# Performance work log

Measured on AMD Instinct MI355X. Metric: run time of the kernel, lower is better.

The kernel has to match this reference:

```python
import jax, jax.numpy as jnp
import numpy as np

NUM_PARTS = 2
SAMPLE_STEP = 3  # models sample_points(pts, 3, True) as deterministic stride-3 subsampling


def quat_to_rot(q):
    # wxyz quaternion -> 3x3 rotation (same formula as the torch module)
    q = q / jnp.linalg.norm(q)
    a, b, c, d = q[0], q[1], q[2], q[3]
    return jnp.stack([
        1 - 2 * c * c - 2 * d * d, 2 * b * c - 2 * a * d, 2 * a * c + 2 * b * d,
        2 * b * c + 2 * a * d, 1 - 2 * b * b - 2 * d * d, 2 * c * d - 2 * a * b,
        2 * b * d - 2 * a * c, 2 * a * b + 2 * c * d, 1 - 2 * b * b - 2 * c * c,
    ]).reshape(3, 3)


def make_transform(q, t):
    rot = quat_to_rot(q)                      # (3,3)
    top = jnp.concatenate([rot, t], axis=1)   # (3,4)
    bottom = jnp.array([[0.0, 0.0, 0.0, 1.0]], dtype=top.dtype)
    return jnp.concatenate([top, bottom], axis=0)  # (4,4)


def chamfer(x, y):
    # x: (M,4), y: (M,4) homogeneous points; symmetric chamfer of Euclidean cdist
    d2 = jnp.sum(x * x, -1)[:, None] + jnp.sum(y * y, -1)[None, :] - 2.0 * (x @ y.T)
    d = jnp.sqrt(jnp.maximum(d2, 0.0))
    return jnp.mean(jnp.min(d, axis=1)) + jnp.mean(jnp.min(d, axis=0))


def setup_inputs() -> dict:
    key = jax.random.key(0)
    ks = jax.random.split(key, 6)
    N = 24576
    camera_pts = jax.random.normal(ks[0], (NUM_PARTS, N, 3), dtype=jnp.float32)
    cad_pts = jax.random.normal(ks[1], (NUM_PARTS, N, 3), dtype=jnp.float32)
    part_weight = jax.random.uniform(ks[2], (NUM_PARTS + 1,), dtype=jnp.float32)
    rot_quat = jax.random.normal(ks[3], (NUM_PARTS, 4), dtype=jnp.float32)
    tra = jax.random.normal(ks[4], (NUM_PARTS, 3, 1), dtype=jnp.float32)
    joint_axes = jax.random.normal(ks[5], (NUM_PARTS, 2, 4), dtype=jnp.float32)
    return {"camera_pts": camera_pts, "cad_pts": cad_pts, "part_weight": part_weight,
            "rot_quat": rot_quat, "tra": tra, "joint_axes": joint_axes}


def reference(camera_pts, cad_pts, part_weight, rot_quat, tra, joint_axes):
    # stride-3 subsample, then homogenize with a ones column
    scad = cad_pts[:, ::SAMPLE_STEP]      # (P, M, 3)
    scam = camera_pts[:, ::SAMPLE_STEP]   # (P, M, 3)
    ones = jnp.ones(scad.shape[:-1] + (1,), dtype=scad.dtype)
    scad_h = jnp.concatenate([scad, ones], axis=-1)  # (P, M, 4)
    scam_h = jnp.concatenate([scam, ones], axis=-1)  # (P, M, 4)

    transforms = jax.vmap(make_transform)(rot_quat, tra)        # (P, 4, 4)
    cad_base = jnp.einsum('pij,pnj->pni', transforms, scad_h)   # (P, M, 4)

    e_geo_parts = jax.vmap(chamfer)(cad_base, scam_h)           # (P,)
    e_geo = jnp.dot(part_weight[:NUM_PARTS], e_geo_parts)

    diff = transforms[0] @ joint_axes[0].T - transforms[1] @ joint_axes[1].T  # (4, K)
    e_kin = jax.nn.sigmoid(-5.0 * jnp.linalg.norm(diff))

    all_objective = e_geo + part_weight[NUM_PARTS] * e_kin
    return all_objective, e_kin, jax.lax.stop_gradient(transforms)
```

## Files before the change

kernel.cpp:

```cpp
#include <hip/hip_runtime.h>
#include <math.h>

#define NS 8192
#define NPTS 24576
#define YSPLIT 16
#define YTILE 512
#define BX 256
#define XPT 4
#define XB (NS / (BX * XPT))


__global__ void prep_kernel(const float* __restrict__ rot_quat,
                            const float* __restrict__ tra,
                            const float* __restrict__ joint_axes,
                            float* __restrict__ ws, float* __restrict__ out) {
    if (threadIdx.x == 0) {
        float T[2][16];
        for (int p = 0; p < 2; ++p) {
            float a = rot_quat[p * 4 + 0], b = rot_quat[p * 4 + 1];
            float c = rot_quat[p * 4 + 2], d = rot_quat[p * 4 + 3];
            float inv = rsqrtf(a * a + b * b + c * c + d * d);
            a *= inv; b *= inv; c *= inv; d *= inv;
            float* t = T[p];
            t[0]  = 1.f - 2.f * c * c - 2.f * d * d;
            t[1]  = 2.f * b * c - 2.f * a * d;
            t[2]  = 2.f * a * c + 2.f * b * d;
            t[3]  = tra[p * 3 + 0];
            t[4]  = 2.f * b * c + 2.f * a * d;
            t[5]  = 1.f - 2.f * b * b - 2.f * d * d;
            t[6]  = 2.f * c * d - 2.f * a * b;
            t[7]  = tra[p * 3 + 1];
            t[8]  = 2.f * b * d - 2.f * a * c;
            t[9]  = 2.f * a * b + 2.f * c * d;
            t[10] = 1.f - 2.f * b * b - 2.f * c * c;
            t[11] = tra[p * 3 + 2];
            t[12] = 0.f; t[13] = 0.f; t[14] = 0.f; t[15] = 1.f;
            for (int k = 0; k < 16; ++k) {
                ws[4 + p * 16 + k] = t[k];
                out[2 + p * 16 + k] = t[k];
            }
        }
        float ss = 0.f;
        for (int i = 0; i < 4; ++i) {
            for (int j = 0; j < 2; ++j) {
                float d0 = 0.f, d1 = 0.f;
                for (int k = 0; k < 4; ++k) {
                    d0 += T[0][i * 4 + k] * joint_axes[0 * 8 + j * 4 + k];
                    d1 += T[1][i * 4 + k] * joint_axes[1 * 8 + j * 4 + k];
                }
                float df = d0 - d1;
                ss += df * df;
            }
        }
        float nrm = sqrtf(ss);
        float ek = 1.f / (1.f + expf(5.f * nrm));
        ws[36] = ek;
        out[1] = ek;
        ws[0] = 0.f; ws[1] = 0.f; ws[2] = 0.f; ws[3] = 0.f;
    }
}

__global__ void pack_kernel(const float* __restrict__ cam_pts,
                            const float* __restrict__ cad_pts,
                            const float* __restrict__ ws,
                            float4* __restrict__ pts) {
    int gid = blockIdx.x * blockDim.x + threadIdx.x;
    if (gid >= 2 * NS) return;
    int p = gid >> 13;
    int i = gid & (NS - 1);
    const float* T = ws + 4 + p * 16;
    int base = p * NPTS * 3 + i * 9;
    float x = cad_pts[base], y = cad_pts[base + 1], z = cad_pts[base + 2];
    float q0 = T[0] * x + T[1] * y + T[2]  * z + T[3];
    float q1 = T[4] * x + T[5] * y + T[6]  * z + T[7];
    float q2 = T[8] * x + T[9] * y + T[10] * z + T[11];
    pts[p * NS + i] = make_float4(q0, q1, q2, q0 * q0 + q1 * q1 + q2 * q2);
    float cx = cam_pts[base], cy = cam_pts[base + 1], cz = cam_pts[base + 2];
    pts[2 * NS + p * NS + i] = make_float4(cx, cy, cz, cx * cx + cy * cy + cz * cz);
}

__global__ __launch_bounds__(BX) void chamfer_kernel(const float4* __restrict__ pts,
                                                     float* __restrict__ partial) {
    int combo = blockIdx.y;
    int p   = combo >> 1;
    int dir = combo & 1;
    const float4* X = pts + (dir == 0 ? p * NS : 2 * NS + p * NS);
    const float4* Y = pts + (dir == 0 ? 2 * NS + p * NS : p * NS);
    int ys = blockIdx.z;
    int xb = blockIdx.x;

    __shared__ float4 sy[YTILE];

    int xbase = xb * (BX * XPT) + threadIdx.x;
    float m0[XPT], m1[XPT], m2[XPT], s[XPT], dmin[XPT];
#pragma unroll
    for (int k = 0; k < XPT; ++k) {
        float4 v = X[xbase + k * BX];
        m0[k] = -2.f * v.x;
        m1[k] = -2.f * v.y;
        m2[k] = -2.f * v.z;
        s[k]  = v.w;
        dmin[k] = 3.4e38f;
    }

    int ybase = ys * YTILE;
    sy[threadIdx.x]       = Y[ybase + threadIdx.x];
    sy[threadIdx.x + BX]  = Y[ybase + BX + threadIdx.x];
    __syncthreads();

#pragma unroll 4
    for (int j = 0; j < YTILE; ++j) {
        float4 y = sy[j];
#pragma unroll
        for (int k = 0; k < XPT; ++k) {
            float d = s[k] + y.w;
            d = fmaf(m0[k], y.x, d);
            d = fmaf(m1[k], y.y, d);
            d = fmaf(m2[k], y.z, d);
            dmin[k] = fminf(dmin[k], d);
        }
    }

#pragma unroll
    for (int k = 0; k < XPT; ++k) {
        partial[combo * (YSPLIT * NS) + ys * NS + xbase + k * BX] = dmin[k];
    }
}

__global__ void reduce_kernel(const float* __restrict__ partial,
                              float* __restrict__ accum) {
    int combo = blockIdx.y;
    int x = blockIdx.x * 256 + threadIdx.x;
    const float* p = partial + combo * (YSPLIT * NS) + x;
    float m = p[0];
#pragma unroll
    for (int ysi = 1; ysi < YSPLIT; ++ysi) m = fminf(m, p[ysi * NS]);
    float d = sqrtf(fmaxf(m, 0.f));
#pragma unroll
    for (int off = 32; off > 0; off >>= 1) d += __shfl_down(d, off, 64);
    __shared__ float sm[4];
    int wid = threadIdx.x >> 6;
    if ((threadIdx.x & 63) == 0) sm[wid] = d;
    __syncthreads();
    if (threadIdx.x == 0) {
        float sum = sm[0] + sm[1] + sm[2] + sm[3];
        atomicAdd(&accum[combo], sum);
    }
}

__global__ void finalize_kernel(const float* __restrict__ ws,
                                const float* __restrict__ pw,
                                float* __restrict__ out) {
    if (threadIdx.x == 0) {
        float e0 = (ws[0] + ws[1]) * (1.f / NS);
        float e1 = (ws[2] + ws[3]) * (1.f / NS);
        float e_geo = pw[0] * e0 + pw[1] * e1;
        out[0] = e_geo + pw[2] * ws[36];
    }
}

extern "C" void kernel_launch(void* const* d_in, const int* in_sizes, int n_in,
                              void* d_out, int out_size, void* d_ws, size_t ws_size,
                              hipStream_t stream) {
    const float* cam = (const float*)d_in[0];
    const float* cad = (const float*)d_in[1];
    const float* pw  = (const float*)d_in[2];
    const float* rq  = (const float*)d_in[3];
    const float* tr  = (const float*)d_in[4];
    const float* ja  = (const float*)d_in[5];
    float* out = (float*)d_out;
    float* ws  = (float*)d_ws;
    float4* pts = (float4*)(ws + 64);
    float* partial = ws + 64 + 16 * NS;

    prep_kernel<<<1, 64, 0, stream>>>(rq, tr, ja, ws, out);
    pack_kernel<<<(2 * NS) / 256, 256, 0, stream>>>(cam, cad, ws, pts);
    dim3 cg(XB, 4, YSPLIT);
    chamfer_kernel<<<cg, BX, 0, stream>>>(pts, partial);
    reduce_kernel<<<dim3(NS / 256, 4), 256, 0, stream>>>(partial, ws);
    finalize_kernel<<<1, 64, 0, stream>>>(ws, pw, out);
}
```

Before: 102.2 us.

## Fuse prep into pack, finalize into reduce, use packed fp32 chamfer math

Each pack thread now builds its transform itself, which removes the separate prep kernel. The finalize step moves into the last reduce block through an atomic completion counter, which removes a second launch. The chamfer inner loop uses 2-wide float vectors so the compiler can emit packed FMA and min instructions. Tiling also changes to 64-thread blocks with 8 x-points each and 64 y-splits. The larger y-split count quadruples the partial buffer that the reduce kernel must read, and the last-block pattern relies on threadfence and atomic ordering.

```diff
diff --git a/kernel.cpp b/kernel.cpp
--- a/kernel.cpp
+++ b/kernel.cpp
@@ -3,84 +3,92 @@
 
 #define NS 8192
 #define NPTS 24576
-#define YSPLIT 16
-#define YTILE 512
-#define BX 256
-#define XPT 4
-#define XB (NS / (BX * XPT))
-
-
-__global__ void prep_kernel(const float* __restrict__ rot_quat,
+
+#define BXC 64
+#define XPT 8
+#define XB (NS / (BXC * XPT))
+#define YSPLIT 64
+#define YTILE (NS / YSPLIT)
+
+#define RB 256
+#define RBLOCKS (4 * (NS / RB))
+
+typedef __attribute__((ext_vector_type(2))) float f32x2;
+
+
+__device__ inline void build_transform(const float* __restrict__ rot_quat,
+                                       const float* __restrict__ tra,
+                                       int p, float* t) {
+    float a = rot_quat[p * 4 + 0], b = rot_quat[p * 4 + 1];
+    float c = rot_quat[p * 4 + 2], d = rot_quat[p * 4 + 3];
+    float inv = rsqrtf(a * a + b * b + c * c + d * d);
+    a *= inv; b *= inv; c *= inv; d *= inv;
+    t[0]  = 1.f - 2.f * c * c - 2.f * d * d;
+    t[1]  = 2.f * b * c - 2.f * a * d;
+    t[2]  = 2.f * a * c + 2.f * b * d;
+    t[3]  = tra[p * 3 + 0];
+    t[4]  = 2.f * b * c + 2.f * a * d;
+    t[5]  = 1.f - 2.f * b * b - 2.f * d * d;
+    t[6]  = 2.f * c * d - 2.f * a * b;
+    t[7]  = tra[p * 3 + 1];
+    t[8]  = 2.f * b * d - 2.f * a * c;
+    t[9]  = 2.f * a * b + 2.f * c * d;
+    t[10] = 1.f - 2.f * b * b - 2.f * c * c;
+    t[11] = tra[p * 3 + 2];
+    t[12] = 0.f; t[13] = 0.f; t[14] = 0.f; t[15] = 1.f;
+}
+
+__global__ void pack_kernel(const float* __restrict__ cam_pts,
+                            const float* __restrict__ cad_pts,
+                            const float* __restrict__ rot_quat,
                             const float* __restrict__ tra,
                             const float* __restrict__ joint_axes,
-                            float* __restrict__ ws, float* __restrict__ out) {
-    if (threadIdx.x == 0) {
-        float T[2][16];
-        for (int p = 0; p < 2; ++p) {
-            float a = rot_quat[p * 4 + 0], b = rot_quat[p * 4 + 1];
-            float c = rot_quat[p * 4 + 2], d = rot_quat[p * 4 + 3];
-            float inv = rsqrtf(a * a + b * b + c * c + d * d);
-            a *= inv; b *= inv; c *= inv; d *= inv;
-            float* t = T[p];
-            t[0]  = 1.f - 2.f * c * c - 2.f * d * d;
-            t[1]  = 2.f * b * c - 2.f * a * d;
-            t[2]  = 2.f * a * c + 2.f * b * d;
-            t[3]  = tra[p * 3 + 0];
-            t[4]  = 2.f * b * c + 2.f * a * d;
-            t[5]  = 1.f - 2.f * b * b - 2.f * d * d;
-            t[6]  = 2.f * c * d - 2.f * a * b;
-            t[7]  = tra[p * 3 + 1];
-            t[8]  = 2.f * b * d - 2.f * a * c;
-            t[9]  = 2.f * a * b + 2.f * c * d;
-            t[10] = 1.f - 2.f * b * b - 2.f * c * c;
-            t[11] = tra[p * 3 + 2];
-            t[12] = 0.f; t[13] = 0.f; t[14] = 0.f; t[15] = 1.f;
-            for (int k = 0; k < 16; ++k) {
-                ws[4 + p * 16 + k] = t[k];
-                out[2 + p * 16 + k] = t[k];
-            }
-        }
+                            float* __restrict__ ws,
+                            float4* __restrict__ pts,
+                            float* __restrict__ out) {
+    int gid = blockIdx.x * blockDim.x + threadIdx.x;
+    int p = gid >> 13;
+    int i = gid & (NS - 1);
+
+    float T[16];
+    build_transform(rot_quat, tra, p, T);
+
+    int base = p * NPTS * 3 + i * 9;
+    float x = cad_pts[base], y = cad_pts[base + 1], z = cad_pts[base + 2];
+    float q0 = fmaf(T[0], x, fmaf(T[1], y, fmaf(T[2],  z, T[3])));
+    float q1 = fmaf(T[4], x, fmaf(T[5], y, fmaf(T[6],  z, T[7])));
+    float q2 = fmaf(T[8], x, fmaf(T[9], y, fmaf(T[10], z, T[11])));
+    pts[p * NS + i] = make_float4(q0, q1, q2, fmaf(q0, q0, fmaf(q1, q1, q2 * q2)));
+    float cx = cam_pts[base], cy = cam_pts[base + 1], cz = cam_pts[base + 2];
+    pts[2 * NS + p * NS + i] =
+        make_float4(cx, cy, cz, fmaf(cx, cx, fmaf(cy, cy, cz * cz)));
+
+    if (gid == 0) {
+        float T0[16], T1[16];
+        build_transform(rot_quat, tra, 0, T0);
+        build_transform(rot_quat, tra, 1, T1);
+        for (int k = 0; k < 16; ++k) { out[2 + k] = T0[k]; out[18 + k] = T1[k]; }
         float ss = 0.f;
-        for (int i = 0; i < 4; ++i) {
+        for (int r = 0; r < 4; ++r)
             for (int j = 0; j < 2; ++j) {
                 float d0 = 0.f, d1 = 0.f;
                 for (int k = 0; k < 4; ++k) {
-                    d0 += T[0][i * 4 + k] * joint_axes[0 * 8 + j * 4 + k];
-                    d1 += T[1][i * 4 + k] * joint_axes[1 * 8 + j * 4 + k];
+                    d0 += T0[r * 4 + k] * joint_axes[j * 4 + k];
+                    d1 += T1[r * 4 + k] * joint_axes[8 + j * 4 + k];
                 }
                 float df = d0 - d1;
                 ss += df * df;
             }
-        }
-        float nrm = sqrtf(ss);
-        float ek = 1.f / (1.f + expf(5.f * nrm));
+        float ek = 1.f / (1.f + expf(5.f * sqrtf(ss)));
         ws[36] = ek;
         out[1] = ek;
         ws[0] = 0.f; ws[1] = 0.f; ws[2] = 0.f; ws[3] = 0.f;
-    }
-}
-
-__global__ void pack_kernel(const float* __restrict__ cam_pts,
-                            const float* __restrict__ cad_pts,
-                            const float* __restrict__ ws,
-                            float4* __restrict__ pts) {
-    int gid = blockIdx.x * blockDim.x + threadIdx.x;
-    if (gid >= 2 * NS) return;
-    int p = gid >> 13;
-    int i = gid & (NS - 1);
-    const float* T = ws + 4 + p * 16;
-    int base = p * NPTS * 3 + i * 9;
-    float x = cad_pts[base], y = cad_pts[base + 1], z = cad_pts[base + 2];
-    float q0 = T[0] * x + T[1] * y + T[2]  * z + T[3];
-    float q1 = T[4] * x + T[5] * y + T[6]  * z + T[7];
-    float q2 = T[8] * x + T[9] * y + T[10] * z + T[11];
-    pts[p * NS + i] = make_float4(q0, q1, q2, q0 * q0 + q1 * q1 + q2 * q2);
-    float cx = cam_pts[base], cy = cam_pts[base + 1], cz = cam_pts[base + 2];
-    pts[2 * NS + p * NS + i] = make_float4(cx, cy, cz, cx * cx + cy * cy + cz * cz);
-}
-
-__global__ __launch_bounds__(BX) void chamfer_kernel(const float4* __restrict__ pts,
-                                                     float* __restrict__ partial) {
+        ((unsigned*)ws)[37] = 0u;
+    }
+}
+
+__global__ __launch_bounds__(BXC) void chamfer_kernel(const float4* __restrict__ pts,
+                                                      float* __restrict__ partial) {
     int combo = blockIdx.y;
     int p   = combo >> 1;
     int dir = combo & 1;
@@ -88,74 +96,86 @@
     const float4* Y = pts + (dir == 0 ? 2 * NS + p * NS : p * NS);
     int ys = blockIdx.z;
     int xb = blockIdx.x;
+    int t  = threadIdx.x;
 
     __shared__ float4 sy[YTILE];
 
-    int xbase = xb * (BX * XPT) + threadIdx.x;
-    float m0[XPT], m1[XPT], m2[XPT], s[XPT], dmin[XPT];
-#pragma unroll
-    for (int k = 0; k < XPT; ++k) {
-        float4 v = X[xbase + k * BX];
-        m0[k] = -2.f * v.x;
-        m1[k] = -2.f * v.y;
-        m2[k] = -2.f * v.z;
-        s[k]  = v.w;
-        dmin[k] = 3.4e38f;
+    int xbase = xb * (BXC * XPT) + t;
+    f32x2 m0[XPT / 2], m1[XPT / 2], m2[XPT / 2], s[XPT / 2], dmin[XPT / 2];
+#pragma unroll
+    for (int g = 0; g < XPT / 2; ++g) {
+        float4 v0 = X[xbase + (2 * g) * BXC];
+        float4 v1 = X[xbase + (2 * g + 1) * BXC];
+        m0[g] = (f32x2){-2.f * v0.x, -2.f * v1.x};
+        m1[g] = (f32x2){-2.f * v0.y, -2.f * v1.y};
+        m2[g] = (f32x2){-2.f * v0.z, -2.f * v1.z};
+        s[g]  = (f32x2){v0.w, v1.w};
+        dmin[g] = (f32x2){3.4e38f, 3.4e38f};
     }
 
     int ybase = ys * YTILE;
-    sy[threadIdx.x]       = Y[ybase + threadIdx.x];
-    sy[threadIdx.x + BX]  = Y[ybase + BX + threadIdx.x];
+#pragma unroll
+    for (int c = 0; c < YTILE / BXC; ++c)
+        sy[t + c * BXC] = Y[ybase + c * BXC + t];
     __syncthreads();
 
 #pragma unroll 4
     for (int j = 0; j < YTILE; ++j) {
         float4 y = sy[j];
-#pragma unroll
-        for (int k = 0; k < XPT; ++k) {
-            float d = s[k] + y.w;
-            d = fmaf(m0[k], y.x, d);
-            d = fmaf(m1[k], y.y, d);
-            d = fmaf(m2[k], y.z, d);
-            dmin[k] = fminf(dmin[k], d);
+        f32x2 yw = (f32x2){y.w, y.w};
+        f32x2 yx = (f32x2){y.x, y.x};
+        f32x2 yy = (f32x2){y.y, y.y};
+        f32x2 yz = (f32x2){y.z, y.z};
+#pragma unroll
+        for (int g = 0; g < XPT / 2; ++g) {
+            f32x2 d = s[g] + yw;
+            d = __builtin_elementwise_fma(m0[g], yx, d);
+            d = __builtin_elementwise_fma(m1[g], yy, d);
+            d = __builtin_elementwise_fma(m2[g], yz, d);
+            dmin[g] = __builtin_elementwise_min(dmin[g], d);
         }
     }
 
-#pragma unroll
-    for (int k = 0; k < XPT; ++k) {
-        partial[combo * (YSPLIT * NS) + ys * NS + xbase + k * BX] = dmin[k];
+    float* prow = partial + (combo * YSPLIT + ys) * NS + xbase;
+#pragma unroll
+    for (int g = 0; g < XPT / 2; ++g) {
+        prow[(2 * g) * BXC]     = dmin[g].x;
+        prow[(2 * g + 1) * BXC] = dmin[g].y;
     }
 }
 
 __global__ void reduce_kernel(const float* __restrict__ partial,
-                              float* __restrict__ accum) {
+                              const float* __restrict__ pw,
+                              float* __restrict__ ws,
+                              float* __restrict__ out) {
     int combo = blockIdx.y;
-    int x = blockIdx.x * 256 + threadIdx.x;
+    int x = blockIdx.x * RB + threadIdx.x;
     const float* p = partial + combo * (YSPLIT * NS) + x;
-    float m = p[0];
-#pragma unroll
-    for (int ysi = 1; ysi < YSPLIT; ++ysi) m = fminf(m, p[ysi * NS]);
+    float m = 3.4e38f;
+#pragma unroll 8
+    for (int ysi = 0; ysi < YSPLIT; ++ysi) m = fminf(m, p[ysi * NS]);
     float d = sqrtf(fmaxf(m, 0.f));
 #pragma unroll
     for (int off = 32; off > 0; off >>= 1) d += __shfl_down(d, off, 64);
-    __shared__ float sm[4];
+    __shared__ float sm[RB / 64];
     int wid = threadIdx.x >> 6;
     if ((threadIdx.x & 63) == 0) sm[wid] = d;
     __syncthreads();
     if (threadIdx.x == 0) {
-        float sum = sm[0] + sm[1] + sm[2] + sm[3];
-        atomicAdd(&accum[combo], sum);
-    }
-}
-
-__global__ void finalize_kernel(const float* __restrict__ ws,
-                                const float* __restrict__ pw,
-                                float* __restrict__ out) {
-    if (threadIdx.x == 0) {
-        float e0 = (ws[0] + ws[1]) * (1.f / NS);
-        float e1 = (ws[2] + ws[3]) * (1.f / NS);
-        float e_geo = pw[0] * e0 + pw[1] * e1;
-        out[0] = e_geo + pw[2] * ws[36];
+        float sum = 0.f;
+        for (int w = 0; w < RB / 64; ++w) sum += sm[w];
+        atomicAdd(&ws[combo], sum);
+        __threadfence();
+        unsigned old = atomicAdd(&((unsigned*)ws)[37], 1u);
+        if (old == RBLOCKS - 1) {
+            float a0 = atomicAdd(&ws[0], 0.f);
+            float a1 = atomicAdd(&ws[1], 0.f);
+            float a2 = atomicAdd(&ws[2], 0.f);
+            float a3 = atomicAdd(&ws[3], 0.f);
+            float e0 = (a0 + a1) * (1.f / NS);
+            float e1 = (a2 + a3) * (1.f / NS);
+            out[0] = pw[0] * e0 + pw[1] * e1 + pw[2] * ws[36];
+        }
     }
 }
 
@@ -173,10 +193,8 @@
     float4* pts = (float4*)(ws + 64);
     float* partial = ws + 64 + 16 * NS;
 
-    prep_kernel<<<1, 64, 0, stream>>>(rq, tr, ja, ws, out);
-    pack_kernel<<<(2 * NS) / 256, 256, 0, stream>>>(cam, cad, ws, pts);
+    pack_kernel<<<(2 * NS) / 256, 256, 0, stream>>>(cam, cad, rq, tr, ja, ws, pts, out);
     dim3 cg(XB, 4, YSPLIT);
-    chamfer_kernel<<<cg, BX, 0, stream>>>(pts, partial);
-    reduce_kernel<<<dim3(NS / 256, 4), 256, 0, stream>>>(partial, ws);
-    finalize_kernel<<<1, 64, 0, stream>>>(ws, pw, out);
-}
+    chamfer_kernel<<<cg, BXC, 0, stream>>>(pts, partial);
+    reduce_kernel<<<dim3(NS / RB, 4), RB, 0, stream>>>(partial, pw, ws, out);
+}
```

New measurement: 108.6 us. +6.3%, slower.
